# Kernel tuning notes

Hardware: AMD Instinct MI355X
Metric: run time of the kernel (lower is better)

Reference implementation:

```python
import jax, jax.numpy as jnp
import numpy as np

GRID, BOXN, LABELN = 14, 2, 20
COORD_RATE, NOOBJ_RATE = 5.0, 0.5
CELL = 1.0 / GRID  # cell_size = 1/grid_num
ALL_BOX = 5 * BOXN


def setup_inputs() -> dict:
    key = jax.random.key(0)
    k1, k2, k3 = jax.random.split(key, 3)
    B = 4096
    C = ALL_BOX + LABELN  # 30
    preds = jax.random.uniform(k1, (B, GRID, GRID, C), dtype=jnp.float32)
    truths = jax.random.uniform(k2, (B, GRID, GRID, C), dtype=jnp.float32)
    objm = jax.random.uniform(k3, (B, GRID, GRID)) < 0.08
    truths = truths.at[..., 4].set(jnp.where(objm, truths[..., 4], 0.0))
    return {"preds": preds, "truths": truths}


def _yolo_loss(preds, truths):
    B = preds.shape[0]
    dt = preds.dtype
    obj = truths[..., 4] > 0                                   # [B,S,S]
    pb = preds[..., :ALL_BOX].reshape(*preds.shape[:3], BOXN, 5)  # [B,S,S,Bx,5]
    tb = truths[..., 0:4]                                       # [B,S,S,4]

    # ---- IoU of every predicted box vs the truth box of its cell ----
    pc = CELL * pb[..., 0:2]; ph = pb[..., 2:4] / 2.0
    tc = CELL * tb[..., 0:2]; th = tb[..., 2:4] / 2.0
    p_lt, p_rb = pc - ph, pc + ph                               # [B,S,S,Bx,2]
    t_lt, t_rb = (tc - th)[..., None, :], (tc + th)[..., None, :]  # [B,S,S,1,2]
    lt = jnp.maximum(p_lt, t_lt)
    rb = jnp.minimum(p_rb, t_rb)
    wh = jnp.clip(rb - lt, 0.0, None)
    inter = wh[..., 0] * wh[..., 1]                             # [B,S,S,Bx]
    pa = (p_rb[..., 0] - p_lt[..., 0]) * (p_rb[..., 1] - p_lt[..., 1])
    ta = (t_rb[..., 0] - t_lt[..., 0]) * (t_rb[..., 1] - t_lt[..., 1])
    ious = inter / (pa + ta - inter)                            # [B,S,S,Bx]

    # ---- responsible-box selection (argmax IoU; ties broken by max conf) ----
    max_iou = jnp.max(ious, axis=-1)                            # [B,S,S]
    tied = ious == max_iou[..., None]
    n_tied = tied.sum(-1)
    conf = pb[..., 4]                                           # [B,S,S,Bx]
    ind_conf = jnp.argmax(jnp.where(tied, conf, -jnp.inf), axis=-1)
    ind_iou = jnp.argmax(ious, axis=-1)
    resp = jnp.where(n_tied > 1, ind_conf, ind_iou)             # [B,S,S]
    resp_oh = jax.nn.one_hot(resp, BOXN, dtype=bool)            # [B,S,S,Bx]

    w_obj = obj.astype(dt)
    pred_resp = jnp.take_along_axis(pb, resp[..., None, None], axis=3)[..., 0, :]  # [B,S,S,5]
    tbox5 = truths[..., 0:5]

    center_loss = jnp.sum(w_obj[..., None] * (pred_resp[..., 0:2] - tbox5[..., 0:2]) ** 2)
    size_loss = jnp.sum(w_obj[..., None] * (jnp.sqrt(pred_resp[..., 2:4]) - jnp.sqrt(tbox5[..., 2:4])) ** 2)
    t_conf = jax.lax.stop_gradient(max_iou)  # .item() in torch detaches the IoU target
    conf_resp_loss = jnp.sum(w_obj * (pred_resp[..., 4] - t_conf) ** 2)
    noresp = (obj[..., None] & (~resp_oh)).astype(dt)
    conf_noresp_loss = jnp.sum(noresp * conf ** 2)
    conf_noobj_loss = jnp.sum((~obj)[..., None].astype(dt) * conf ** 2)
    label_loss = jnp.sum(w_obj[..., None] * (preds[..., ALL_BOX:] - truths[..., ALL_BOX:]) ** 2)

    return (COORD_RATE * (center_loss + size_loss) + conf_resp_loss
            + NOOBJ_RATE * conf_noresp_loss + NOOBJ_RATE * conf_noobj_loss
            + label_loss) / B


def reference(preds, truths):
    return _yolo_loss(preds, truths)
```

## Files before the change

kernel.cpp:

```cpp
#include <hip/hip_runtime.h>
#include <math.h>

#define GRIDN   14
#define BOXN    2
#define LABELN  20
#define ALL_BOX 10
#define CCH     30

#define TCELLS  64
#define TF4     480
#define VTOT    960
#define PBLOCKS 2048

typedef float vfloat4 __attribute__((ext_vector_type(4)));

__global__ void yolo_zero_kernel(float* out, int n) {
    int i = blockIdx.x * blockDim.x + threadIdx.x;
    if (i < n) out[i] = 0.0f;
}

__device__ __forceinline__ float cell_loss(const float* p, const float* t) {
#pragma clang fp contract(off)
    const float CELL = (float)(1.0 / (double)GRIDN);

    const float tx = t[0], ty = t[1], tw = t[2], th_ = t[3], tconf = t[4];
    const bool obj = tconf > 0.0f;

    const float tcx = CELL * tx, tcy = CELL * ty;
    const float thx = tw * 0.5f, thy = th_ * 0.5f;
    const float tltx = tcx - thx, tlty = tcy - thy;
    const float trbx = tcx + thx, trby = tcy + thy;
    const float ta = (trbx - tltx) * (trby - tlty);

    float iou[BOXN], conf[BOXN];
#pragma unroll
    for (int b = 0; b < BOXN; ++b) {
        const float bx = p[b * 5 + 0], by = p[b * 5 + 1];
        const float bw = p[b * 5 + 2], bh = p[b * 5 + 3];
        conf[b] = p[b * 5 + 4];
        const float pcx = CELL * bx, pcy = CELL * by;
        const float phx = bw * 0.5f, phy = bh * 0.5f;
        const float pltx = pcx - phx, plty = pcy - phy;
        const float prbx = pcx + phx, prby = pcy + phy;
        const float ltx = fmaxf(pltx, tltx), lty = fmaxf(plty, tlty);
        const float rbx = fminf(prbx, trbx), rby = fminf(prby, trby);
        const float whx = fmaxf(rbx - ltx, 0.0f);
        const float why = fmaxf(rby - lty, 0.0f);
        const float inter = whx * why;
        const float pa = (prbx - pltx) * (prby - plty);
        iou[b] = inter / (pa + ta - inter);
    }

    const float max_iou = fmaxf(iou[0], iou[1]);
    bool r1;
    if (iou[0] == iou[1]) r1 = !(conf[0] >= conf[1]);
    else                  r1 = !(iou[0] > iou[1]);

    const float rx = r1 ? p[5] : p[0];
    const float ry = r1 ? p[6] : p[1];
    const float rw = r1 ? p[7] : p[2];
    const float rh = r1 ? p[8] : p[3];
    const float rc = r1 ? p[9] : p[4];

    const float dcx = rx - tx;
    const float dcy = ry - ty;
    const float center = dcx * dcx + dcy * dcy;

    const float dsx = sqrtf(rw) - sqrtf(tw);
    const float dsy = sqrtf(rh) - sqrtf(th_);
    const float size = dsx * dsx + dsy * dsy;

    const float dconf = rc - max_iou;
    const float conf_resp = dconf * dconf;

    const float c_other = r1 ? conf[0] : conf[1];
    const float conf_noresp = c_other * c_other;

    const float conf_noobj = conf[0] * conf[0] + conf[1] * conf[1];

    float label = 0.0f;
#pragma unroll
    for (int k = ALL_BOX; k < CCH; ++k) {
        const float d = p[k] - t[k];
        label += d * d;
    }

    const float w  = obj ? 1.0f : 0.0f;
    const float nw = obj ? 0.0f : 1.0f;
    return w * (5.0f * (center + size) + conf_resp + 0.5f * conf_noresp + label)
         + nw * (0.5f * conf_noobj);
}

__global__ __launch_bounds__(256, 8) void yolo_loss_kernel(
    const float* __restrict__ preds,
    const float* __restrict__ truths,
    float* __restrict__ out,
    int ntiles)
{
#pragma clang fp contract(off)
    __shared__ vfloat4 sbuf[VTOT];

    const int tid = threadIdx.x;

    const vfloat4* pp = (const vfloat4*)preds;
    const vfloat4* tp = (const vfloat4*)truths;

    vfloat4 R[4];
    int tile = blockIdx.x;

    if (tile < ntiles) {
        const int g = tile * TF4;
#pragma unroll
        for (int i = 0; i < 4; ++i) {
            const int idx = i * 256 + tid;
            if (idx < VTOT)
                R[i] = (idx < TF4) ? pp[g + idx] : tp[g + (idx - TF4)];
        }
    }

    float acc = 0.0f;
    for (; tile < ntiles; tile += PBLOCKS) {
        const int next = tile + PBLOCKS;

        __syncthreads();
#pragma unroll
        for (int i = 0; i < 4; ++i) {
            const int idx = i * 256 + tid;
            if (idx < VTOT) sbuf[idx] = R[i];
        }

        if (next < ntiles) {
            const int g = next * TF4;
#pragma unroll
            for (int i = 0; i < 4; ++i) {
                const int idx = i * 256 + tid;
                if (idx < VTOT)
                    R[i] = (idx < TF4) ? pp[g + idx] : tp[g + (idx - TF4)];
            }
        }
        __syncthreads();

        if (tid < TCELLS) {
            const float* sf = (const float*)sbuf;
            acc += cell_loss(sf + tid * CCH, sf + TF4 * 4 + tid * CCH);
        }
    }

    if (tid < 64) {
#pragma unroll
        for (int off = 32; off > 0; off >>= 1) acc += __shfl_down(acc, off, 64);
        if (tid == 0) atomicAdd(out, acc * (1.0f / 4096.0f));
    }
}

extern "C" void kernel_launch(void* const* d_in, const int* in_sizes, int n_in,
                              void* d_out, int out_size, void* d_ws, size_t ws_size,
                              hipStream_t stream) {
    const float* preds  = (const float*)d_in[0];
    const float* truths = (const float*)d_in[1];
    float* out = (float*)d_out;

    const int ncells = in_sizes[0] / CCH;
    const int ntiles = ncells / TCELLS;

    yolo_zero_kernel<<<(out_size + 255) / 256, 256, 0, stream>>>(out, out_size);
    yolo_loss_kernel<<<PBLOCKS, 256, 0, stream>>>(preds, truths, out, ntiles);
}
```

Measured before the change: 212.4 us.

## Stream tiles directly into LDS with a four-buffer async global_load_lds pipeline

Replaces the register-staged single-buffer load with direct global-to-LDS async loads (global_load_lds) into four rotating LDS buffers, keeping three tiles in flight per block. Waits use explicit vmcnt counts per wave plus a raw s_barrier. Block count drops to 512 with launch bounds lowered to two blocks per CU, to fit the larger LDS footprint. The aim is deeper memory-level parallelism and no VGPR round trip, at the cost of lower occupancy and fragile hand-counted vmcnt/barrier ordering. The buffer being refilled was last read in the previous iteration, and only the barrier guards that reuse.

```diff
diff --git a/kernel.cpp b/kernel.cpp
--- a/kernel.cpp
+++ b/kernel.cpp
@@ -10,7 +10,9 @@
 #define TCELLS  64
 #define TF4     480
 #define VTOT    960
-#define PBLOCKS 2048
+#define NBUF    4
+#define NCHUNK  4
+#define PBLOCKS 512
 
 typedef float vfloat4 __attribute__((ext_vector_type(4)));
 
@@ -91,59 +93,65 @@
          + nw * (0.5f * conf_noobj);
 }
 
-__global__ __launch_bounds__(256, 8) void yolo_loss_kernel(
+#define WAITV(n) asm volatile("s_waitcnt vmcnt(" #n ")" ::: "memory")
+
+__global__ __launch_bounds__(256, 2) void yolo_loss_kernel(
     const float* __restrict__ preds,
     const float* __restrict__ truths,
     float* __restrict__ out,
     int ntiles)
 {
 #pragma clang fp contract(off)
-    __shared__ vfloat4 sbuf[VTOT];
+    __shared__ vfloat4 sbuf[NBUF * VTOT];
 
-    const int tid = threadIdx.x;
+    const int tid   = threadIdx.x;
+    const int wave  = tid >> 6;
+    const int wbase = tid & ~63;
 
     const vfloat4* pp = (const vfloat4*)preds;
     const vfloat4* tp = (const vfloat4*)truths;
 
-    vfloat4 R[4];
-    int tile = blockIdx.x;
+#define STAGE(tt, b)                                                         \
+    do {                                                                     \
+        const int gb_ = (tt) * TF4;                                          \
+        _Pragma("unroll")                                                    \
+        for (int i_ = 0; i_ < NCHUNK; ++i_) {                                \
+            const int cb_ = i_ * 256 + wbase;                                \
+            if (cb_ < VTOT) {                                                \
+                const int v_ = i_ * 256 + tid;                               \
+                const vfloat4* src_ = (v_ < TF4) ? (pp + gb_ + v_)           \
+                                                 : (tp + gb_ + (v_ - TF4));  \
+                __builtin_amdgcn_global_load_lds(                            \
+                    (const __attribute__((address_space(1))) void*)src_,     \
+                    (__attribute__((address_space(3))) void*)                \
+                        (sbuf + (b) * VTOT + cb_),                           \
+                    16, 0, 0);                                               \
+            }                                                                \
+        }                                                                    \
+    } while (0)
 
-    if (tile < ntiles) {
-        const int g = tile * TF4;
-#pragma unroll
-        for (int i = 0; i < 4; ++i) {
-            const int idx = i * 256 + tid;
-            if (idx < VTOT)
-                R[i] = (idx < TF4) ? pp[g + idx] : tp[g + (idx - TF4)];
-        }
-    }
+    int t = blockIdx.x;
+    if (t < ntiles)               STAGE(t, 0);
+    if (t + PBLOCKS < ntiles)     STAGE(t + PBLOCKS, 1);
+    if (t + 2 * PBLOCKS < ntiles) STAGE(t + 2 * PBLOCKS, 2);
 
     float acc = 0.0f;
-    for (; tile < ntiles; tile += PBLOCKS) {
-        const int next = tile + PBLOCKS;
+    int k = 0;
+    for (; t < ntiles; t += PBLOCKS, ++k) {
+        const int a = (t + PBLOCKS < ntiles) + (t + 2 * PBLOCKS < ntiles);
 
-        __syncthreads();
-#pragma unroll
-        for (int i = 0; i < 4; ++i) {
-            const int idx = i * 256 + tid;
-            if (idx < VTOT) sbuf[idx] = R[i];
-        }
+        if (a == 2)      { if (wave < 3) WAITV(8); else WAITV(6); }
+        else if (a == 1) { if (wave < 3) WAITV(4); else WAITV(3); }
+        else             { WAITV(0); }
+        __builtin_amdgcn_s_barrier();
+        __builtin_amdgcn_sched_barrier(0);
 
-        if (next < ntiles) {
-            const int g = next * TF4;
-#pragma unroll
-            for (int i = 0; i < 4; ++i) {
-                const int idx = i * 256 + tid;
-                if (idx < VTOT)
-                    R[i] = (idx < TF4) ? pp[g + idx] : tp[g + (idx - TF4)];
-            }
-        }
-        __syncthreads();
+        const int t3 = t + 3 * PBLOCKS;
+        if (t3 < ntiles) STAGE(t3, (k + 3) & 3);
 
-        if (tid < TCELLS) {
-            const float* sf = (const float*)sbuf;
+        const float* sf = (const float*)(sbuf + (k & 3) * VTOT);
+        if (tid < TCELLS)
             acc += cell_loss(sf + tid * CCH, sf + TF4 * 4 + tid * CCH);
-        }
     }
 
     if (tid < 64) {
```

Result: faster. 208.1 us (-2.0%).
